# Kernel optimization log

Measured on AMD Instinct MI355X. Metric: run time of the kernel, lower is better.

Reference implementation:

```python
import jax, jax.numpy as jnp
import numpy as np
from jax import lax

D_MODEL = 1024
D_STATE = 16
EXPAND = 2
KERNEL = 4
BATCH = 4
SEQ = 4096
LN_EPS = 1e-5


def _ln(x, w, b):
    m = jnp.mean(x, axis=-1, keepdims=True)
    v = jnp.mean((x - m) ** 2, axis=-1, keepdims=True)
    return (x - m) * lax.rsqrt(v + LN_EPS) * w + b


def setup_inputs() -> dict:
    key = jax.random.key(0)
    ks = jax.random.split(key, 16)
    d, n, e, k = D_MODEL, D_STATE, EXPAND, KERNEL

    def lin(key, fan_in, shape):
        bound = 1.0 / np.sqrt(fan_in)
        return jax.random.uniform(key, shape, jnp.float32, -bound, bound)

    return {
        "x": jax.random.normal(ks[0], (BATCH, SEQ, d), jnp.float32),
        "ln1_w": jnp.ones((d,), jnp.float32),
        "ln1_b": jnp.zeros((d,), jnp.float32),
        "conv_w": lin(ks[1], k, (d, 1, k)),  # depthwise conv, groups=d -> fan_in=k
        "conv_b": lin(ks[2], k, (d,)),
        "lns_w": jnp.ones((d,), jnp.float32),
        "lns_b": jnp.zeros((d,), jnp.float32),
        "in_w": lin(ks[3], d, (d, 2 * d)),
        "in_b": lin(ks[4], d, (2 * d,)),
        "xp_w": lin(ks[5], d, (d, n)),
        "xp_b": lin(ks[6], d, (n,)),
        "A_log": jax.random.normal(ks[7], (n,), jnp.float32),
        "D": jax.random.normal(ks[8], (n, d), jnp.float32),
        "out_w": lin(ks[9], d, (d, d)),
        "out_b": lin(ks[10], d, (d,)),
        "ln2_w": jnp.ones((d,), jnp.float32),
        "ln2_b": jnp.zeros((d,), jnp.float32),
        "mlp_w1": lin(ks[11], d, (d, e * d)),
        "mlp_b1": lin(ks[12], d, (e * d,)),
        "mlp_w2": lin(ks[13], e * d, (e * d, d)),
        "mlp_b2": lin(ks[14], e * d, (d,)),
    }


def reference(x, ln1_w, ln1_b, conv_w, conv_b, lns_w, lns_b, in_w, in_b,
              xp_w, xp_b, A_log, D, out_w, out_b, ln2_w, ln2_b,
              mlp_w1, mlp_b1, mlp_w2, mlp_b2):
    b, s, d = x.shape
    # --- depthwise causal-padded conv branch (truncated to seq_len) ---
    xn = _ln(x, ln1_w, ln1_b)
    xc = jnp.transpose(xn, (0, 2, 1))  # (b, d, s)
    xc = lax.conv_general_dilated(
        xc, conv_w, window_strides=(1,), padding=[(KERNEL - 1, KERNEL - 1)],
        feature_group_count=d, dimension_numbers=("NCH", "OIH", "NCH"))
    xc = xc + conv_b[None, :, None]
    xc = jnp.transpose(xc, (0, 2, 1))[:, :s]  # (b, s, d)
    x = x + xc

    # --- SelectiveScanLayer ---
    residual = x
    xn = _ln(x, lns_w, lns_b)
    xz = xn @ in_w + in_b
    xp, z = jnp.split(xz, 2, axis=-1)
    xp = jax.nn.silu(xp)
    z = jax.nn.sigmoid(z)
    u = xp @ xp_w + xp_b  # (b, s, n)
    decay = jnp.exp(-jnp.exp(A_log))  # exp(A), A = -exp(A_log); (n,)

    u_t = jnp.transpose(u, (1, 0, 2))  # (s, b, n)

    def step(h, u_i):
        h = decay * h + u_i
        return h, h

    _, hs = lax.scan(step, jnp.zeros((b, D_STATE), x.dtype), u_t)  # (s, b, n)
    ys = jnp.einsum("sbn,nd->sbd", hs, D) * jnp.transpose(z, (1, 0, 2))
    ys = ys @ out_w + out_b  # (s, b, d)
    # faithful to original: torch stack gives (1,s,b,d), then .view(b,s,d)
    y = ys.reshape(b, s, d)
    x = residual + y

    # --- MLP (dropout inactive at eval) ---
    h = _ln(x, ln2_w, ln2_b)
    h = jax.nn.gelu(h @ mlp_w1 + mlp_b1, approximate=False)
    h = h @ mlp_w2 + mlp_b2
    return x + h
```

## Files before the change

kernel.cpp:

```cpp
#include <hip/hip_runtime.h>
#include <cstdint>
#include <cstddef>


typedef short bf16x8 __attribute__((ext_vector_type(8)));
typedef float f32x4 __attribute__((ext_vector_type(4)));

#define GLD16(gp, lp)                                                          \
  __builtin_amdgcn_global_load_lds(                                            \
      (__attribute__((address_space(1))) void*)(gp),                           \
      (__attribute__((address_space(3))) void*)(lp), 16, 0, 0)

static __device__ __forceinline__ ushort f2bf(float f) {
  union { float f; uint32_t u; } c; c.f = f;
  uint32_t r = c.u + 0x7FFFu + ((c.u >> 16) & 1u);
  return (ushort)(r >> 16);
}
static __device__ __forceinline__ float bf2f(ushort u) {
  union { uint32_t u; float f; } c; c.u = ((uint32_t)u) << 16;
  return c.f;
}

__global__ __launch_bounds__(256) void rowstats_kernel(
    const float* __restrict__ x, float2* __restrict__ stats) {
  const int row = blockIdx.x * 4 + (threadIdx.x >> 6);
  const int lane = threadIdx.x & 63;
  const float4* xr = (const float4*)(x + (size_t)row * 1024);
  float s = 0.f, q = 0.f;
#pragma unroll
  for (int i = 0; i < 4; i++) {
    const float4 v = xr[lane + i * 64];
    s += v.x + v.y + v.z + v.w;
    q += v.x * v.x + v.y * v.y + v.z * v.z + v.w * v.w;
  }
#pragma unroll
  for (int off = 32; off > 0; off >>= 1) {
    s += __shfl_down(s, off);
    q += __shfl_down(q, off);
  }
  if (lane == 0) {
    const float mean = s * (1.f / 1024.f);
    const float var  = q * (1.f / 1024.f) - mean * mean;
    stats[row] = make_float2(mean, rsqrtf(var + 1e-5f));
  }
}

__global__ __launch_bounds__(256) void lnconv_kernel(
    const float* __restrict__ x, const float2* __restrict__ stats,
    const float* __restrict__ ln1w, const float* __restrict__ ln1b,
    const float* __restrict__ cw, const float* __restrict__ cb,
    const float* __restrict__ lnsw, const float* __restrict__ lnsb,
    float* __restrict__ x1, ushort* __restrict__ abuf) {
  const int row = blockIdx.x * 4 + (threadIdx.x >> 6);
  const int t = row & 4095;
  const int lane = threadIdx.x & 63;
  const float4* x4 = (const float4*)x;

  float2 st[4];
#pragma unroll
  for (int j = 0; j < 4; j++)
    st[j] = (t - 3 + j >= 0) ? stats[row - 3 + j] : make_float2(0.f, 0.f);

  float4 o[4];
  float s = 0.f, q = 0.f;
#pragma unroll
  for (int i = 0; i < 4; i++) {
    const int f4 = lane + i * 64;
    const int c0 = f4 * 4;
    float4 acc = *(const float4*)(cb + c0);
    const float4 w0 = *(const float4*)(cw + (size_t)(c0 + 0) * 4);
    const float4 w1 = *(const float4*)(cw + (size_t)(c0 + 1) * 4);
    const float4 w2 = *(const float4*)(cw + (size_t)(c0 + 2) * 4);
    const float4 w3 = *(const float4*)(cw + (size_t)(c0 + 3) * 4);
    const float4 wv4 = ((const float4*)ln1w)[f4];
    const float4 bv4 = ((const float4*)ln1b)[f4];
    float4 xm = make_float4(0.f, 0.f, 0.f, 0.f);
#pragma unroll
    for (int j = 0; j < 4; j++) {
      if (t - 3 + j >= 0) {
        const float4 xv = x4[(size_t)(row - 3 + j) * 256 + f4];
        if (j == 3) xm = xv;
        const float mean = st[j].x, rstd = st[j].y;
        const float lx = (xv.x - mean) * rstd * wv4.x + bv4.x;
        const float ly = (xv.y - mean) * rstd * wv4.y + bv4.y;
        const float lz = (xv.z - mean) * rstd * wv4.z + bv4.z;
        const float lw = (xv.w - mean) * rstd * wv4.w + bv4.w;
        acc.x += lx * ((const float*)&w0)[j];
        acc.y += ly * ((const float*)&w1)[j];
        acc.z += lz * ((const float*)&w2)[j];
        acc.w += lw * ((const float*)&w3)[j];
      }
    }
    o[i].x = xm.x + acc.x; o[i].y = xm.y + acc.y;
    o[i].z = xm.z + acc.z; o[i].w = xm.w + acc.w;
    ((float4*)x1)[(size_t)row * 256 + f4] = o[i];
    s += o[i].x + o[i].y + o[i].z + o[i].w;
    q += o[i].x * o[i].x + o[i].y * o[i].y + o[i].z * o[i].z + o[i].w * o[i].w;
  }
#pragma unroll
  for (int off = 1; off < 64; off <<= 1) {
    s += __shfl_xor(s, off);
    q += __shfl_xor(q, off);
  }
  const float mean = s * (1.f / 1024.f);
  const float var  = q * (1.f / 1024.f) - mean * mean;
  const float rstd = rsqrtf(var + 1e-5f);
#pragma unroll
  for (int i = 0; i < 4; i++) {
    const int f4 = lane + i * 64;
    const float4 wv4 = ((const float4*)lnsw)[f4];
    const float4 bv4 = ((const float4*)lnsb)[f4];
    ushort4 a;
    a.x = f2bf((o[i].x - mean) * rstd * wv4.x + bv4.x);
    a.y = f2bf((o[i].y - mean) * rstd * wv4.y + bv4.y);
    a.z = f2bf((o[i].z - mean) * rstd * wv4.z + bv4.z);
    a.w = f2bf((o[i].w - mean) * rstd * wv4.w + bv4.w);
    ((ushort4*)(abuf + (size_t)row * 1024))[f4] = a;
  }
}

template <int BF16OUT>
__global__ __launch_bounds__(256) void ln_kernel(
    const float* __restrict__ x, const float* __restrict__ w,
    const float* __restrict__ b, void* __restrict__ out) {
  const int row = blockIdx.x * 4 + (threadIdx.x >> 6);
  const int lane = threadIdx.x & 63;
  const float4* xr = (const float4*)(x + (size_t)row * 1024);
  float4 v[4];
  float s = 0.f, q = 0.f;
#pragma unroll
  for (int i = 0; i < 4; i++) {
    v[i] = xr[lane + i * 64];
    s += v[i].x + v[i].y + v[i].z + v[i].w;
    q += v[i].x * v[i].x + v[i].y * v[i].y + v[i].z * v[i].z + v[i].w * v[i].w;
  }
#pragma unroll
  for (int off = 1; off < 64; off <<= 1) {
    s += __shfl_xor(s, off);
    q += __shfl_xor(q, off);
  }
  const float mean = s * (1.f / 1024.f);
  const float var  = q * (1.f / 1024.f) - mean * mean;
  const float rstd = rsqrtf(var + 1e-5f);
#pragma unroll
  for (int i = 0; i < 4; i++) {
    const int f4 = lane + i * 64;
    const float4 wv4 = ((const float4*)w)[f4];
    const float4 bv4 = ((const float4*)b)[f4];
    const float o0 = (v[i].x - mean) * rstd * wv4.x + bv4.x;
    const float o1 = (v[i].y - mean) * rstd * wv4.y + bv4.y;
    const float o2 = (v[i].z - mean) * rstd * wv4.z + bv4.z;
    const float o3 = (v[i].w - mean) * rstd * wv4.w + bv4.w;
    if (BF16OUT) {
      ushort4 o; o.x = f2bf(o0); o.y = f2bf(o1); o.z = f2bf(o2); o.w = f2bf(o3);
      ((ushort4*)((ushort*)out + (size_t)row * 1024))[f4] = o;
    } else {
      float4 o; o.x = o0; o.y = o1; o.z = o2; o.w = o3;
      ((float4*)((float*)out + (size_t)row * 1024))[f4] = o;
    }
  }
}

__global__ __launch_bounds__(256) void wt_all_kernel(
    const float* __restrict__ in_w, const float* __restrict__ out_w,
    const float* __restrict__ w1, const float* __restrict__ w2,
    ushort* __restrict__ in_wT, ushort* __restrict__ out_wT,
    ushort* __restrict__ w1T, ushort* __restrict__ w2T) {
  __shared__ float tile[32][33];
  const int idx = blockIdx.x;
  const float* src; ushort* dst; int K, N, n0, k0;
  if (idx < 2048) {
    src = in_w; dst = in_wT; K = 1024; N = 2048;
    n0 = (idx & 63) * 32; k0 = (idx >> 6) * 32;
  } else if (idx < 3072) {
    const int r = idx - 2048;
    src = out_w; dst = out_wT; K = 1024; N = 1024;
    n0 = (r & 31) * 32; k0 = (r >> 5) * 32;
  } else if (idx < 5120) {
    const int r = idx - 3072;
    src = w1; dst = w1T; K = 1024; N = 2048;
    n0 = (r & 63) * 32; k0 = (r >> 6) * 32;
  } else {
    const int r = idx - 5120;
    src = w2; dst = w2T; K = 2048; N = 1024;
    n0 = (r & 31) * 32; k0 = (r >> 5) * 32;
  }
  const int tx = threadIdx.x & 31, ty = threadIdx.x >> 5;
#pragma unroll
  for (int j = 0; j < 32; j += 8)
    tile[ty + j][tx] = src[(size_t)(k0 + ty + j) * N + n0 + tx];
  __syncthreads();
#pragma unroll
  for (int j = 0; j < 32; j += 8)
    dst[(size_t)(n0 + ty + j) * K + k0 + tx] = f2bf(tile[tx][ty + j]);
}

__global__ __launch_bounds__(256) void u_mfma_kernel(
    const ushort* __restrict__ xp, const float* __restrict__ xpw,
    const float* __restrict__ xpb, float* __restrict__ u) {
  __shared__ ushort Ws[16 * 1024];
  __shared__ ushort As[64 * 64];
  const int tid = threadIdx.x;
  const int wave = tid >> 6, lane = tid & 63;
  const int l16 = lane & 15, quad = lane >> 4;
  for (int e = tid; e < 16384; e += 256) {
    const int n = e & 15, k = e >> 4;
    Ws[n * 1024 + (((k >> 3) ^ (n & 7)) << 3) + (k & 7)] =
        f2bf(xpw[(size_t)k * 16 + n]);
  }
  const int bm0 = blockIdx.x * 64;
  const int srow = lane >> 3, sblk = (lane & 7) ^ (srow & 7);
  const ushort* Ag = xp + (size_t)(bm0 + wave * 16 + srow) * 1024 + sblk * 8;
  ushort* Al = &As[wave * 16 * 64];
  const int rsw = l16 & 7;
  f32x4 acc = (f32x4){0.f, 0.f, 0.f, 0.f};
  __syncthreads();
  for (int k0 = 0; k0 < 1024; k0 += 64) {
    GLD16(Ag + k0, Al);
    GLD16(Ag + k0 + (size_t)8 * 1024, Al + 512);
    __syncthreads();
#pragma unroll
    for (int kh = 0; kh < 2; kh++) {
      const bf16x8 aF = *(const bf16x8*)
          &As[(wave * 16 + l16) * 64 + (((kh * 4 + quad) ^ rsw) << 3)];
      const bf16x8 bF = *(const bf16x8*)
          &Ws[l16 * 1024 + ((((k0 >> 3) + kh * 4 + quad) ^ rsw) << 3)];
      acc = __builtin_amdgcn_mfma_f32_16x16x32_bf16(aF, bF, acc, 0, 0, 0);
    }
    __syncthreads();
  }
  const float bv = xpb[l16];
#pragma unroll
  for (int r = 0; r < 4; r++) {
    const int row = bm0 + wave * 16 + quad * 4 + r;
    u[(size_t)row * 16 + l16] = acc[r] + bv;
  }
}

__global__ __launch_bounds__(256) void scan_kernel(
    const float* __restrict__ u, const float* __restrict__ A_log,
    float* __restrict__ hs) {
  const int tid = threadIdx.x;
  const int b = blockIdx.x >> 4;
  const int n = blockIdx.x & 15;
  const float d = expf(-expf(A_log[n]));
  const int t0 = tid * 16;
  const float* up = u + ((size_t)b * 4096) * 16 + n;
  float loc[16];
  float h = 0.f;
#pragma unroll
  for (int i = 0; i < 16; i++) {
    h = d * h + up[(size_t)(t0 + i) * 16];
    loc[i] = h;
  }
  __shared__ float sv[256];
  sv[tid] = h;
  __syncthreads();
  float d16 = d * d; d16 *= d16; d16 *= d16; d16 *= d16;
  float f = d16;
  for (int off = 1; off < 256; off <<= 1) {
    const float add = (tid >= off) ? sv[tid - off] : 0.f;
    __syncthreads();
    sv[tid] += f * add;
    __syncthreads();
    f *= f;
  }
  const float carry = (tid > 0) ? sv[tid - 1] : 0.f;
  float dp = d;
#pragma unroll
  for (int i = 0; i < 16; i++) {
    const float hg = loc[i] + dp * carry;
    dp *= d;
    hs[((size_t)(t0 + i) * 4 + b) * 16 + n] = hg;
  }
}

__global__ __launch_bounds__(256) void g_kernel(
    const float* __restrict__ hs, const float* __restrict__ Dm,
    const ushort* __restrict__ z, ushort* __restrict__ g) {
  __shared__ float hsh[256];
  const int tid = threadIdx.x;
  const int r0 = blockIdx.x * 16;
  hsh[tid] = hs[(size_t)r0 * 16 + tid];
  __syncthreads();
  float4 acc[16];
#pragma unroll
  for (int rr = 0; rr < 16; rr++) acc[rr] = make_float4(0.f, 0.f, 0.f, 0.f);
  const float4* Dv = (const float4*)Dm;
#pragma unroll
  for (int n = 0; n < 16; n++) {
    const float4 dv = Dv[(size_t)n * 256 + tid];
#pragma unroll
    for (int rr = 0; rr < 16; rr++) {
      const float h = hsh[rr * 16 + n];
      acc[rr].x += h * dv.x; acc[rr].y += h * dv.y;
      acc[rr].z += h * dv.z; acc[rr].w += h * dv.w;
    }
  }
#pragma unroll
  for (int rr = 0; rr < 16; rr++) {
    const int r = r0 + rr;
    const int b = r & 3, t = r >> 2;
    const ushort4 zv =
        *(const ushort4*)(z + ((size_t)b * 4096 + t) * 1024 + tid * 4);
    ushort4 o;
    o.x = f2bf(acc[rr].x * bf2f(zv.x)); o.y = f2bf(acc[rr].y * bf2f(zv.y));
    o.z = f2bf(acc[rr].z * bf2f(zv.z)); o.w = f2bf(acc[rr].w * bf2f(zv.w));
    *(ushort4*)(g + (size_t)r * 1024 + tid * 4) = o;
  }
}

template <int EPI>
__global__ __launch_bounds__(512, 2) void gemm_bt(
    const ushort* __restrict__ A, const ushort* __restrict__ Bt,
    const float* __restrict__ bias, int K, void* __restrict__ p0,
    void* __restrict__ p1) {
  __shared__ __align__(16) ushort sm[65536];
  const int tid = threadIdx.x;
  const int wave = tid >> 6, lane = tid & 63;
  const int l16 = lane & 15, quad = lane >> 4;
  const int wm = wave >> 2, wn = wave & 3;

  const int nbx = (int)gridDim.x;
  int tm, tn;
  if ((nbx & 7) == 0) {
    const int lid = (int)blockIdx.y * nbx + (int)blockIdx.x;
    const int ncm = nbx >> 3;
    const int xcd = lid & 7;
    const int j = lid >> 3;
    tm = xcd * ncm + (j % ncm);
    tn = j / ncm;
  } else {
    tm = (int)blockIdx.x; tn = (int)blockIdx.y;
  }
  const int bm0 = tm * 256, bn0 = tn * 256;

  const int srow = lane >> 3;
  const int sblk = (lane & 7) ^ srow;
  const int NT = K >> 6;

  const ushort* Astg = A + (size_t)(bm0 + wave * 8 + srow) * K + sblk * 8;
  const ushort* Bstg = Bt + (size_t)(bn0 + wave * 8 + srow) * K + sblk * 8;

#define SA(i, kt, base)                                                        \
  GLD16(Astg + (size_t)((i) * 64) * K + (kt) * 64,                             \
        &sm[(base) + (i) * 4096 + wave * 512])
#define SB(i, kt, base)                                                        \
  GLD16(Bstg + (size_t)((i) * 64) * K + (kt) * 64,                             \
        &sm[(base) + 16384 + (i) * 4096 + wave * 512])

  const int rsw = l16 & 7;
  const int c80 = (quad ^ rsw) << 3;
  const int c81 = ((4 + quad) ^ rsw) << 3;
  const int aoff = (wm * 128 + l16) * 64;
  const int boff = 16384 + (wn * 64 + l16) * 64;

  f32x4 acc[8][4];
#pragma unroll
  for (int i = 0; i < 8; i++)
#pragma unroll
    for (int j = 0; j < 4; j++) acc[i][j] = (f32x4){0.f, 0.f, 0.f, 0.f};

#pragma unroll
  for (int i = 0; i < 4; i++) { SA(i, 0, 0); SB(i, 0, 0); }
  if (NT > 1) {
#pragma unroll
    for (int i = 0; i < 4; i++) { SA(i, 1, 32768); SB(i, 1, 32768); }
    asm volatile("s_waitcnt vmcnt(8)" ::: "memory");
  } else {
    asm volatile("s_waitcnt vmcnt(0)" ::: "memory");
  }
  __builtin_amdgcn_s_barrier();

  bf16x8 af[4][2], b01[2][2], b23[2][2];

  for (int t = 0; t < NT; ++t) {
    const int cb = (t & 1) << 15;
#pragma unroll
    for (int i = 0; i < 4; i++) {
      af[i][0] = *(const bf16x8*)&sm[cb + aoff + i * 1024 + c80];
      af[i][1] = *(const bf16x8*)&sm[cb + aoff + i * 1024 + c81];
    }
#pragma unroll
    for (int j = 0; j < 2; j++) {
      b01[j][0] = *(const bf16x8*)&sm[cb + boff + j * 1024 + c80];
      b01[j][1] = *(const bf16x8*)&sm[cb + boff + j * 1024 + c81];
    }
    __builtin_amdgcn_s_barrier();
    asm volatile("s_waitcnt lgkmcnt(0)" ::: "memory");
    __builtin_amdgcn_sched_barrier(0);
    __builtin_amdgcn_s_setprio(1);
#pragma unroll
    for (int i = 0; i < 4; i++)
#pragma unroll
      for (int j = 0; j < 2; j++) {
        acc[i][j] = __builtin_amdgcn_mfma_f32_16x16x32_bf16(
            b01[j][0], af[i][0], acc[i][j], 0, 0, 0);
        acc[i][j] = __builtin_amdgcn_mfma_f32_16x16x32_bf16(
            b01[j][1], af[i][1], acc[i][j], 0, 0, 0);
      }
    __builtin_amdgcn_s_setprio(0);
    __builtin_amdgcn_s_barrier();
#pragma unroll
    for (int j = 0; j < 2; j++) {
      b23[j][0] = *(const bf16x8*)&sm[cb + boff + (2 + j) * 1024 + c80];
      b23[j][1] = *(const bf16x8*)&sm[cb + boff + (2 + j) * 1024 + c81];
    }
    __builtin_amdgcn_s_barrier();
    asm volatile("s_waitcnt lgkmcnt(0)" ::: "memory");
    __builtin_amdgcn_sched_barrier(0);
    __builtin_amdgcn_s_setprio(1);
#pragma unroll
    for (int i = 0; i < 4; i++)
#pragma unroll
      for (int j = 0; j < 2; j++) {
        acc[i][2 + j] = __builtin_amdgcn_mfma_f32_16x16x32_bf16(
            b23[j][0], af[i][0], acc[i][2 + j], 0, 0, 0);
        acc[i][2 + j] = __builtin_amdgcn_mfma_f32_16x16x32_bf16(
            b23[j][1], af[i][1], acc[i][2 + j], 0, 0, 0);
      }
    __builtin_amdgcn_s_setprio(0);
    __builtin_amdgcn_s_barrier();
#pragma unroll
    for (int i = 0; i < 4; i++) {
      af[i][0] = *(const bf16x8*)&sm[cb + aoff + (4 + i) * 1024 + c80];
      af[i][1] = *(const bf16x8*)&sm[cb + aoff + (4 + i) * 1024 + c81];
    }
    __builtin_amdgcn_s_barrier();
    asm volatile("s_waitcnt lgkmcnt(0)" ::: "memory");
    __builtin_amdgcn_sched_barrier(0);
    __builtin_amdgcn_s_setprio(1);
#pragma unroll
    for (int i = 0; i < 4; i++)
#pragma unroll
      for (int j = 0; j < 2; j++) {
        acc[4 + i][j] = __builtin_amdgcn_mfma_f32_16x16x32_bf16(
            b01[j][0], af[i][0], acc[4 + i][j], 0, 0, 0);
        acc[4 + i][j] = __builtin_amdgcn_mfma_f32_16x16x32_bf16(
            b01[j][1], af[i][1], acc[4 + i][j], 0, 0, 0);
      }
    __builtin_amdgcn_s_setprio(0);
    __builtin_amdgcn_s_barrier();
    if (t + 2 < NT) {
#pragma unroll
      for (int i = 0; i < 4; i++) { SA(i, t + 2, cb); SB(i, t + 2, cb); }
    }
    __builtin_amdgcn_s_setprio(1);
#pragma unroll
    for (int i = 0; i < 4; i++)
#pragma unroll
      for (int j = 0; j < 2; j++) {
        acc[4 + i][2 + j] = __builtin_amdgcn_mfma_f32_16x16x32_bf16(
            b23[j][0], af[i][0], acc[4 + i][2 + j], 0, 0, 0);
        acc[4 + i][2 + j] = __builtin_amdgcn_mfma_f32_16x16x32_bf16(
            b23[j][1], af[i][1], acc[4 + i][2 + j], 0, 0, 0);
      }
    __builtin_amdgcn_s_setprio(0);
    if (t + 2 < NT) {
      asm volatile("s_waitcnt vmcnt(8)" ::: "memory");
    } else {
      asm volatile("s_waitcnt vmcnt(0)" ::: "memory");
    }
    __builtin_amdgcn_s_barrier();
  }
#undef SA
#undef SB

#pragma unroll
  for (int i = 0; i < 8; i++) {
    const size_t row = (size_t)(bm0 + wm * 128 + i * 16 + l16);
#pragma unroll
    for (int j = 0; j < 4; j++) {
      const int c = bn0 + wn * 64 + j * 16 + quad * 4;
      const float4 bv = *(const float4*)(bias + c);
      const float v0 = acc[i][j][0] + bv.x;
      const float v1 = acc[i][j][1] + bv.y;
      const float v2 = acc[i][j][2] + bv.z;
      const float v3 = acc[i][j][3] + bv.w;
      if (EPI == 0) {
        ushort4 o;
        if (c < 1024) {
          o.x = f2bf(v0 / (1.f + __expf(-v0)));
          o.y = f2bf(v1 / (1.f + __expf(-v1)));
          o.z = f2bf(v2 / (1.f + __expf(-v2)));
          o.w = f2bf(v3 / (1.f + __expf(-v3)));
          *(ushort4*)((ushort*)p0 + row * 1024 + c) = o;
        } else {
          o.x = f2bf(1.f / (1.f + __expf(-v0)));
          o.y = f2bf(1.f / (1.f + __expf(-v1)));
          o.z = f2bf(1.f / (1.f + __expf(-v2)));
          o.w = f2bf(1.f / (1.f + __expf(-v3)));
          *(ushort4*)((ushort*)p1 + row * 1024 + (c - 1024)) = o;
        }
      } else if (EPI == 1) {
        float4* io = (float4*)((float*)p0 + row * 1024 + c);
        float4 t4 = *io;
        t4.x += v0; t4.y += v1; t4.z += v2; t4.w += v3;
        *io = t4;
      } else if (EPI == 2) {
        ushort4 o;
        o.x = f2bf(0.5f * v0 * (1.f + erff(v0 * 0.70710678118654752f)));
        o.y = f2bf(0.5f * v1 * (1.f + erff(v1 * 0.70710678118654752f)));
        o.z = f2bf(0.5f * v2 * (1.f + erff(v2 * 0.70710678118654752f)));
        o.w = f2bf(0.5f * v3 * (1.f + erff(v3 * 0.70710678118654752f)));
        *(ushort4*)((ushort*)p0 + row * 2048 + c) = o;
      } else {
        const float4 pv = *(const float4*)((const float*)p1 + row * 1024 + c);
        float4 t4;
        t4.x = pv.x + v0; t4.y = pv.y + v1;
        t4.z = pv.z + v2; t4.w = pv.w + v3;
        *(float4*)((float*)p0 + row * 1024 + c) = t4;
      }
    }
  }
}

extern "C" void kernel_launch(void* const* d_in, const int* in_sizes, int n_in,
                              void* d_out, int out_size, void* d_ws,
                              size_t ws_size, hipStream_t stream) {
  const float* x      = (const float*)d_in[0];
  const float* ln1_w  = (const float*)d_in[1];
  const float* ln1_b  = (const float*)d_in[2];
  const float* conv_w = (const float*)d_in[3];
  const float* conv_b = (const float*)d_in[4];
  const float* lns_w  = (const float*)d_in[5];
  const float* lns_b  = (const float*)d_in[6];
  const float* in_w   = (const float*)d_in[7];
  const float* in_b   = (const float*)d_in[8];
  const float* xp_w   = (const float*)d_in[9];
  const float* xp_b   = (const float*)d_in[10];
  const float* A_log  = (const float*)d_in[11];
  const float* Dm     = (const float*)d_in[12];
  const float* out_w  = (const float*)d_in[13];
  const float* out_b  = (const float*)d_in[14];
  const float* ln2_w  = (const float*)d_in[15];
  const float* ln2_b  = (const float*)d_in[16];
  const float* mlp_w1 = (const float*)d_in[17];
  const float* mlp_b1 = (const float*)d_in[18];
  const float* mlp_w2 = (const float*)d_in[19];
  const float* mlp_b2 = (const float*)d_in[20];

  char* wsp = (char*)d_ws;
  size_t off = 0;
  auto alloc = [&](size_t bytes) {
    void* p = wsp + off;
    off += (bytes + 255) & ~(size_t)255;
    return p;
  };
  float*  x1    = (float*)alloc(67108864);
  ushort* abuf  = (ushort*)alloc(67108864);
  ushort* gbuf  = abuf + 16777216;
  ushort* xpb   = (ushort*)alloc(33554432);
  ushort* zb    = (ushort*)alloc(67108864);
  ushort* h1b   = (ushort*)zb;
  float*  ub    = (float*)alloc(1048576);
  float*  hsb   = (float*)alloc(1048576);
  float2* stb   = (float2*)alloc(131072);
  ushort* in_wT = (ushort*)alloc(4194304);
  ushort* out_wT= (ushort*)alloc(2097152);
  ushort* w1T   = (ushort*)alloc(4194304);
  ushort* w2T   = (ushort*)alloc(4194304);

  wt_all_kernel<<<7168, 256, 0, stream>>>(in_w, out_w, mlp_w1, mlp_w2,
                                          in_wT, out_wT, w1T, w2T);
  rowstats_kernel<<<4096, 256, 0, stream>>>(x, stb);
  lnconv_kernel<<<4096, 256, 0, stream>>>(x, stb, ln1_w, ln1_b, conv_w,
                                          conv_b, lns_w, lns_b, x1, abuf);
  gemm_bt<0><<<dim3(64, 8), 512, 0, stream>>>(abuf, in_wT, in_b, 1024,
                                              xpb, zb);
  u_mfma_kernel<<<256, 256, 0, stream>>>(xpb, xp_w, xp_b, ub);
  scan_kernel<<<64, 256, 0, stream>>>(ub, A_log, hsb);
  g_kernel<<<1024, 256, 0, stream>>>(hsb, Dm, zb, gbuf);
  gemm_bt<1><<<dim3(64, 4), 512, 0, stream>>>(gbuf, out_wT, out_b, 1024,
                                              x1, nullptr);
  ln_kernel<1><<<4096, 256, 0, stream>>>(x1, ln2_w, ln2_b, xpb);
  gemm_bt<2><<<dim3(64, 8), 512, 0, stream>>>(xpb, w1T, mlp_b1, 1024,
                                              h1b, nullptr);
  gemm_bt<3><<<dim3(64, 4), 512, 0, stream>>>(h1b, w2T, mlp_b2, 2048,
                                              d_out, x1);
}
```

Measured before the change: 638.4 us.

## Simplify GEMM main loop to two compute phases with fewer barriers

Replaces the four-phase ping-pong GEMM inner loop, which had explicit barriers, sched_barriers and setprio around each MFMA cluster, with a simpler two-half loop. All B fragments are loaded once per k-tile, and the compiler is left free to interleave LDS reads with MFMAs. The next-tile global-to-LDS prefetch now issues after all MFMAs. This removes several barriers per iteration, but holding B fragments for the whole iteration raises register pressure, and the loss of priority scheduling and of prefetch overlap with the last MFMA block may hurt.

```diff
diff --git a/kernel.cpp b/kernel.cpp
--- a/kernel.cpp
+++ b/kernel.cpp
@@ -371,97 +371,56 @@
     asm volatile("s_waitcnt vmcnt(0)" ::: "memory");
   }
   __builtin_amdgcn_s_barrier();
-
-  bf16x8 af[4][2], b01[2][2], b23[2][2];
+  asm volatile("" ::: "memory");
 
   for (int t = 0; t < NT; ++t) {
     const int cb = (t & 1) << 15;
+    bf16x8 af[4][2], bfr[4][2];
+#pragma unroll
+    for (int j = 0; j < 4; j++) {
+      bfr[j][0] = *(const bf16x8*)&sm[cb + boff + j * 1024 + c80];
+      bfr[j][1] = *(const bf16x8*)&sm[cb + boff + j * 1024 + c81];
+    }
 #pragma unroll
     for (int i = 0; i < 4; i++) {
       af[i][0] = *(const bf16x8*)&sm[cb + aoff + i * 1024 + c80];
       af[i][1] = *(const bf16x8*)&sm[cb + aoff + i * 1024 + c81];
     }
 #pragma unroll
-    for (int j = 0; j < 2; j++) {
-      b01[j][0] = *(const bf16x8*)&sm[cb + boff + j * 1024 + c80];
-      b01[j][1] = *(const bf16x8*)&sm[cb + boff + j * 1024 + c81];
-    }
-    __builtin_amdgcn_s_barrier();
-    asm volatile("s_waitcnt lgkmcnt(0)" ::: "memory");
-    __builtin_amdgcn_sched_barrier(0);
-    __builtin_amdgcn_s_setprio(1);
-#pragma unroll
     for (int i = 0; i < 4; i++)
 #pragma unroll
-      for (int j = 0; j < 2; j++) {
+      for (int j = 0; j < 4; j++) {
         acc[i][j] = __builtin_amdgcn_mfma_f32_16x16x32_bf16(
-            b01[j][0], af[i][0], acc[i][j], 0, 0, 0);
+            bfr[j][0], af[i][0], acc[i][j], 0, 0, 0);
         acc[i][j] = __builtin_amdgcn_mfma_f32_16x16x32_bf16(
-            b01[j][1], af[i][1], acc[i][j], 0, 0, 0);
+            bfr[j][1], af[i][1], acc[i][j], 0, 0, 0);
       }
-    __builtin_amdgcn_s_setprio(0);
-    __builtin_amdgcn_s_barrier();
-#pragma unroll
-    for (int j = 0; j < 2; j++) {
-      b23[j][0] = *(const bf16x8*)&sm[cb + boff + (2 + j) * 1024 + c80];
-      b23[j][1] = *(const bf16x8*)&sm[cb + boff + (2 + j) * 1024 + c81];
-    }
-    __builtin_amdgcn_s_barrier();
-    asm volatile("s_waitcnt lgkmcnt(0)" ::: "memory");
-    __builtin_amdgcn_sched_barrier(0);
-    __builtin_amdgcn_s_setprio(1);
-#pragma unroll
-    for (int i = 0; i < 4; i++)
-#pragma unroll
-      for (int j = 0; j < 2; j++) {
-        acc[i][2 + j] = __builtin_amdgcn_mfma_f32_16x16x32_bf16(
-            b23[j][0], af[i][0], acc[i][2 + j], 0, 0, 0);
-        acc[i][2 + j] = __builtin_amdgcn_mfma_f32_16x16x32_bf16(
-            b23[j][1], af[i][1], acc[i][2 + j], 0, 0, 0);
-      }
-    __builtin_amdgcn_s_setprio(0);
-    __builtin_amdgcn_s_barrier();
 #pragma unroll
     for (int i = 0; i < 4; i++) {
       af[i][0] = *(const bf16x8*)&sm[cb + aoff + (4 + i) * 1024 + c80];
       af[i][1] = *(const bf16x8*)&sm[cb + aoff + (4 + i) * 1024 + c81];
     }
+#pragma unroll
+    for (int i = 0; i < 4; i++)
+#pragma unroll
+      for (int j = 0; j < 4; j++) {
+        acc[4 + i][j] = __builtin_amdgcn_mfma_f32_16x16x32_bf16(
+            bfr[j][0], af[i][0], acc[4 + i][j], 0, 0, 0);
+        acc[4 + i][j] = __builtin_amdgcn_mfma_f32_16x16x32_bf16(
+            bfr[j][1], af[i][1], acc[4 + i][j], 0, 0, 0);
+      }
+    asm volatile("s_waitcnt lgkmcnt(0)" ::: "memory");
     __builtin_amdgcn_s_barrier();
-    asm volatile("s_waitcnt lgkmcnt(0)" ::: "memory");
-    __builtin_amdgcn_sched_barrier(0);
-    __builtin_amdgcn_s_setprio(1);
-#pragma unroll
-    for (int i = 0; i < 4; i++)
-#pragma unroll
-      for (int j = 0; j < 2; j++) {
-        acc[4 + i][j] = __builtin_amdgcn_mfma_f32_16x16x32_bf16(
-            b01[j][0], af[i][0], acc[4 + i][j], 0, 0, 0);
-        acc[4 + i][j] = __builtin_amdgcn_mfma_f32_16x16x32_bf16(
-            b01[j][1], af[i][1], acc[4 + i][j], 0, 0, 0);
-      }
-    __builtin_amdgcn_s_setprio(0);
-    __builtin_amdgcn_s_barrier();
+    asm volatile("" ::: "memory");
     if (t + 2 < NT) {
 #pragma unroll
       for (int i = 0; i < 4; i++) { SA(i, t + 2, cb); SB(i, t + 2, cb); }
-    }
-    __builtin_amdgcn_s_setprio(1);
-#pragma unroll
-    for (int i = 0; i < 4; i++)
-#pragma unroll
-      for (int j = 0; j < 2; j++) {
-        acc[4 + i][2 + j] = __builtin_amdgcn_mfma_f32_16x16x32_bf16(
-            b23[j][0], af[i][0], acc[4 + i][2 + j], 0, 0, 0);
-        acc[4 + i][2 + j] = __builtin_amdgcn_mfma_f32_16x16x32_bf16(
-            b23[j][1], af[i][1], acc[4 + i][2 + j], 0, 0, 0);
-      }
-    __builtin_amdgcn_s_setprio(0);
-    if (t + 2 < NT) {
       asm volatile("s_waitcnt vmcnt(8)" ::: "memory");
     } else {
       asm volatile("s_waitcnt vmcnt(0)" ::: "memory");
     }
     __builtin_amdgcn_s_barrier();
+    asm volatile("" ::: "memory");
   }
 #undef SA
 #undef SB
```

Measured after the change: 628.4 us. About the same (-1.6%).
